# Optimization experiments

Measured on AMD Instinct MI355X. Metric: run time of the kernel, lower is better.

Reference implementation:

```python
import jax, jax.numpy as jnp
import numpy as np

N_NODES = 50000
N_EDGES = 800000
IN_FEATS = 256
OUT_FEATS = 64


def setup_inputs() -> dict:
    key = jax.random.key(0)
    k1, k2, k3, k4 = jax.random.split(key, 4)
    feat = jax.random.normal(k1, (N_NODES, IN_FEATS), dtype=jnp.float32)
    src = jax.random.randint(k2, (N_EDGES,), 0, N_NODES, dtype=jnp.int32)
    dst = jax.random.randint(k3, (N_EDGES,), 0, N_NODES, dtype=jnp.int32)
    # Glorot-uniform like DGL's GraphConv weight init
    limit = float(np.sqrt(6.0 / (IN_FEATS + OUT_FEATS)))
    W = jax.random.uniform(k4, (IN_FEATS, OUT_FEATS), dtype=jnp.float32,
                           minval=-limit, maxval=limit)
    b = jnp.zeros((OUT_FEATS,), dtype=jnp.float32)
    return {"feat": feat, "src": src, "dst": dst, "W": W, "b": b}


def reference(feat, src, dst, W, b):
    n = feat.shape[0]
    ones = jnp.ones_like(src, dtype=feat.dtype)
    out_deg = jax.ops.segment_sum(ones, src, num_segments=n)
    in_deg = jax.ops.segment_sum(ones, dst, num_segments=n)
    # norm='both': deg^{-1/2}, degrees clamped to min 1 (allow_zero_in_degree)
    norm_src = jax.lax.rsqrt(jnp.maximum(out_deg, 1.0))   # [N]
    norm_dst = jax.lax.rsqrt(jnp.maximum(in_deg, 1.0))    # [N]
    # in_feats > out_feats -> apply weight before aggregation (DGL fast path)
    h = (feat * norm_src[:, None]) @ W                    # [N, out]
    agg = jax.ops.segment_sum(h[src], dst, num_segments=n)  # SpMM: sum messages at dst
    rst = agg * norm_dst[:, None] + b
    return jax.nn.sigmoid(rst)
```

## Files before the change

### kernel.cpp

```cpp
#include <hip/hip_runtime.h>
#include <hip/hip_bf16.h>
#include <math.h>

#define N_NODES 50000
#define N_EDGES 800000
#define IN_F 256
#define OUT_F 64

#define BKT 256
#define NB 196
#define CAP 6144
#define PARTA_BLOCKS 400
#define EPB (N_EDGES / PARTA_BLOCKS)
#define GEMM_BM 32

typedef __attribute__((ext_vector_type(8))) short bf16x8;
typedef __attribute__((ext_vector_type(4))) float f32x4;

__device__ __forceinline__ ushort f2bf(float x) {
    __hip_bfloat16 b = __float2bfloat16(x);
    return *reinterpret_cast<ushort*>(&b);
}
__device__ __forceinline__ float bf_lo(uint v) { return __uint_as_float(v << 16); }
__device__ __forceinline__ float bf_hi(uint v) { return __uint_as_float(v & 0xffff0000u); }

__global__ __launch_bounds__(256) void prep_kernel(int* __restrict__ bcnt,
                                                   const float* __restrict__ W,
                                                   ushort* __restrict__ Wpk) {
    const int tid = threadIdx.x;
    if (blockIdx.x == 0) {
        for (int i = tid; i < 2 * NB; i += 256) bcnt[i] = 0;
    } else {
        const int gid = (blockIdx.x - 1) * 256 + tid;
        const int lane = gid & 63;
        const int ct = (gid >> 6) & 3;
        const int step = gid >> 8;
        const int kg = lane >> 4;
        const int n = lane & 15;
        const float* base = W + (size_t)(step * 32 + kg * 8) * OUT_F + ct * 16 + n;
        union { ushort u[8]; uint4 v; } pk;
        #pragma unroll
        for (int j = 0; j < 8; ++j) pk.u[j] = f2bf(base[(size_t)j * OUT_F]);
        ((uint4*)Wpk)[gid] = pk.v;
    }
}

__global__ __launch_bounds__(512) void partA_kernel(const int* __restrict__ src,
                                                    const int* __restrict__ dst,
                                                    int* __restrict__ bcntD,
                                                    int* __restrict__ bcntS,
                                                    uint* __restrict__ pairsD,
                                                    ushort* __restrict__ srcloc) {
    __shared__ int lcntD[NB], lbaseD[NB], lcntS[NB], lbaseS[NB];
    const int tid = threadIdx.x;
    const int n4 = EPB / 4;

    for (int i = tid; i < NB; i += 512) { lcntD[i] = 0; lcntS[i] = 0; }
    __syncthreads();

    const int4* t4 = (const int4*)(dst + (size_t)blockIdx.x * EPB);
    const int4* s4 = (const int4*)(src + (size_t)blockIdx.x * EPB);

    for (int i = tid; i < n4; i += 512) {
        const int4 d = t4[i];
        const int4 s = s4[i];
        atomicAdd(&lcntD[d.x >> 8], 1); atomicAdd(&lcntS[s.x >> 8], 1);
        atomicAdd(&lcntD[d.y >> 8], 1); atomicAdd(&lcntS[s.y >> 8], 1);
        atomicAdd(&lcntD[d.z >> 8], 1); atomicAdd(&lcntS[s.z >> 8], 1);
        atomicAdd(&lcntD[d.w >> 8], 1); atomicAdd(&lcntS[s.w >> 8], 1);
    }
    __syncthreads();

    for (int i = tid; i < NB; i += 512) {
        int c = lcntD[i];
        lbaseD[i] = c ? atomicAdd(&bcntD[i], c) : 0;
        lcntD[i] = 0;
        c = lcntS[i];
        lbaseS[i] = c ? atomicAdd(&bcntS[i], c) : 0;
        lcntS[i] = 0;
    }
    __syncthreads();

    for (int i = tid; i < n4; i += 512) {
        const int4 d = t4[i];
        const int4 s = s4[i];
        int bx, off;
        #define PLACE(dd, ss)                                                  \
            bx = (dd) >> 8; off = atomicAdd(&lcntD[bx], 1);                    \
            pairsD[(size_t)bx * CAP + lbaseD[bx] + off] =                      \
                ((uint)((dd) & 255) << 16) | (uint)(ss);                       \
            bx = (ss) >> 8; off = atomicAdd(&lcntS[bx], 1);                    \
            srcloc[(size_t)bx * CAP + lbaseS[bx] + off] = (ushort)((ss) & 255);
        PLACE(d.x, s.x)
        PLACE(d.y, s.y)
        PLACE(d.z, s.z)
        PLACE(d.w, s.w)
        #undef PLACE
    }
}

__global__ __launch_bounds__(1024) void bucket_kernel(const ushort* __restrict__ srcloc,
                                                      const int* __restrict__ bcntS,
                                                      float* __restrict__ normS,
                                                      const uint* __restrict__ pairsD,
                                                      const int* __restrict__ bcntD,
                                                      int* __restrict__ ptr,
                                                      int* __restrict__ indeg,
                                                      ushort* __restrict__ sorted_src) {
    __shared__ int cnt[BKT];
    __shared__ int loff[BKT];
    __shared__ int wtot[4];
    const int bb = blockIdx.x;
    const int tid = threadIdx.x;
    const int node = bb * BKT + tid;

    if (tid < BKT) cnt[tid] = 0;
    __syncthreads();
    const int nS = bcntS[bb];
    const ushort* sp = srcloc + (size_t)bb * CAP;
    for (int i = tid; i < nS; i += 1024) atomicAdd(&cnt[sp[i]], 1);
    __syncthreads();
    if (tid < BKT && node < N_NODES)
        normS[node] = rsqrtf(fmaxf((float)cnt[tid], 1.0f));
    __syncthreads();

    if (tid < BKT) cnt[tid] = 0;
    __syncthreads();
    const int nD = bcntD[bb];
    const uint* pb = pairsD + (size_t)bb * CAP;
    for (int i = tid; i < nD; i += 1024) atomicAdd(&cnt[pb[i] >> 16], 1);
    __syncthreads();

    if (tid < BKT) {
        const int lane = tid & 63;
        const int wave = tid >> 6;
        const int v = cnt[tid];
        int incl = v;
        #pragma unroll
        for (int d = 1; d < 64; d <<= 1) {
            int u = __shfl_up(incl, d, 64);
            if (lane >= d) incl += u;
        }
        if (lane == 63) wtot[wave] = incl;
        loff[tid] = incl - v;
    }
    __syncthreads();
    if (tid < BKT) {
        const int wave = tid >> 6;
        int woff = 0;
        #pragma unroll
        for (int w = 0; w < 4; ++w)
            if (w < wave) woff += wtot[w];
        const int ex = woff + loff[tid];
        loff[tid] = ex;
        const int v = cnt[tid];
        cnt[tid] = 0;
        if (node < N_NODES) { ptr[node] = bb * CAP + ex; indeg[node] = v; }
    }
    __syncthreads();

    for (int i = tid; i < nD; i += 1024) {
        const uint p = pb[i];
        const int local = (int)(p >> 16);
        const int pos = atomicAdd(&cnt[local], 1);
        sorted_src[(size_t)bb * CAP + loff[local] + pos] = (ushort)(p & 0xFFFFu);
    }
}

__global__ __launch_bounds__(256) void gemm_kernel(const float* __restrict__ feat,
                                                   const ushort* __restrict__ Wpk,
                                                   ushort* __restrict__ h) {
    __shared__ float ftile[GEMM_BM * IN_F];
    const int tid = threadIdx.x;
    const int lane = tid & 63;
    const int wave = tid >> 6;
    const int m = lane & 15;
    const int g = lane >> 4;
    const int rowBase = blockIdx.x * GEMM_BM;
    const char* fb = (const char*)feat;

    #pragma unroll
    for (int it = 0; it < 8; ++it) {
        const int R = it * 4 + wave;
        const int off = (lane * 16) ^ ((R & 7) << 4);
        int grow = rowBase + R;
        if (grow >= N_NODES) grow = N_NODES - 1;
        __builtin_amdgcn_global_load_lds(
            (const __attribute__((address_space(1))) void*)(fb + ((size_t)grow << 10) + off),
            (__attribute__((address_space(3))) void*)((char*)ftile + it * 4096 + wave * 1024),
            16, 0, 0);
    }
    __syncthreads();

    const int rowHalf = wave & 1;
    const int colHalf = wave >> 1;

    f32x4 acc[2];
    acc[0] = (f32x4){0.f, 0.f, 0.f, 0.f};
    acc[1] = (f32x4){0.f, 0.f, 0.f, 0.f};

    const int Rr = rowHalf * 16 + m;
    const int swz = (Rr & 7) << 4;
    const char* rowb = (const char*)ftile + (Rr << 10);
    const bf16x8* wp = (const bf16x8*)Wpk;

    #pragma unroll
    for (int step = 0; step < 8; ++step) {
        const int kb = step * 128 + g * 32;
        const float4 a0 = *(const float4*)(rowb + (kb ^ swz));
        const float4 a1 = *(const float4*)(rowb + ((kb + 16) ^ swz));
        bf16x8 aa;
        aa[0] = (short)f2bf(a0.x); aa[1] = (short)f2bf(a0.y);
        aa[2] = (short)f2bf(a0.z); aa[3] = (short)f2bf(a0.w);
        aa[4] = (short)f2bf(a1.x); aa[5] = (short)f2bf(a1.y);
        aa[6] = (short)f2bf(a1.z); aa[7] = (short)f2bf(a1.w);
        #pragma unroll
        for (int ct = 0; ct < 2; ++ct)
            acc[ct] = __builtin_amdgcn_mfma_f32_16x16x32_bf16(
                aa, wp[(step * 4 + colHalf * 2 + ct) * 64 + lane], acc[ct], 0, 0, 0);
    }

    #pragma unroll
    for (int j = 0; j < 4; ++j) {
        const int row = rowBase + rowHalf * 16 + g * 4 + j;
        if (row < N_NODES) {
            #pragma unroll
            for (int ct = 0; ct < 2; ++ct)
                h[(size_t)row * OUT_F + colHalf * 32 + ct * 16 + m] = f2bf(acc[ct][j]);
        }
    }
}

__global__ __launch_bounds__(256) void gather_kernel(const int* __restrict__ ptr,
                                                     const int* __restrict__ indeg,
                                                     const ushort* __restrict__ sorted_src,
                                                     const float* __restrict__ normS,
                                                     const ushort* __restrict__ h,
                                                     const float* __restrict__ b,
                                                     float* __restrict__ out) {
    const int lane = threadIdx.x & 63;
    const int q = lane & 15;
    const int g = lane >> 4;
    int nid = (int)((blockIdx.x * (size_t)blockDim.x + threadIdx.x) >> 6);
    if (nid >= N_NODES) return;
    nid = __builtin_amdgcn_readfirstlane(nid);

    const int beg = ptr[nid];
    const int deg = indeg[nid];

    float a0 = 0.f, a1 = 0.f, a2 = 0.f, a3 = 0.f;
    const int nfull = deg >> 2;
    int e = beg + g;
    #pragma unroll 4
    for (int i = 0; i < nfull; ++i) {
        const int s = (int)sorted_src[e];
        e += 4;
        const float ns = normS[s];
        const uint2 v = *(const uint2*)(h + (size_t)s * OUT_F + q * 4);
        a0 = fmaf(ns, bf_lo(v.x), a0); a1 = fmaf(ns, bf_hi(v.x), a1);
        a2 = fmaf(ns, bf_lo(v.y), a2); a3 = fmaf(ns, bf_hi(v.y), a3);
    }
    const int rem = deg & 3;
    if (g < rem) {
        const int s = (int)sorted_src[beg + (deg & ~3) + g];
        const float ns = normS[s];
        const uint2 v = *(const uint2*)(h + (size_t)s * OUT_F + q * 4);
        a0 = fmaf(ns, bf_lo(v.x), a0); a1 = fmaf(ns, bf_hi(v.x), a1);
        a2 = fmaf(ns, bf_lo(v.y), a2); a3 = fmaf(ns, bf_hi(v.y), a3);
    }
    a0 += __shfl_xor(a0, 16, 64); a1 += __shfl_xor(a1, 16, 64);
    a2 += __shfl_xor(a2, 16, 64); a3 += __shfl_xor(a3, 16, 64);
    a0 += __shfl_xor(a0, 32, 64); a1 += __shfl_xor(a1, 32, 64);
    a2 += __shfl_xor(a2, 32, 64); a3 += __shfl_xor(a3, 32, 64);

    if (g == 0) {
        const float norm = rsqrtf(fmaxf((float)deg, 1.0f));
        const float4 bb = *(const float4*)(b + q * 4);
        float4 o;
        o.x = 1.0f / (1.0f + expf(-(a0 * norm + bb.x)));
        o.y = 1.0f / (1.0f + expf(-(a1 * norm + bb.y)));
        o.z = 1.0f / (1.0f + expf(-(a2 * norm + bb.z)));
        o.w = 1.0f / (1.0f + expf(-(a3 * norm + bb.w)));
        *(float4*)(out + (size_t)nid * OUT_F + q * 4) = o;
    }
}

extern "C" void kernel_launch(void* const* d_in, const int* in_sizes, int n_in,
                              void* d_out, int out_size, void* d_ws, size_t ws_size,
                              hipStream_t stream) {
    const float* feat = (const float*)d_in[0];
    const int* src    = (const int*)d_in[1];
    const int* dst    = (const int*)d_in[2];
    const float* W    = (const float*)d_in[3];
    const float* b    = (const float*)d_in[4];
    float* out = (float*)d_out;

    char* ws = (char*)d_ws;
    size_t off = 0;
    ushort* h = (ushort*)(ws + off);        off += (size_t)N_NODES * OUT_F * 2;
    float* normS = (float*)(ws + off);      off += (size_t)N_NODES * 4;
    int* indeg = (int*)(ws + off);          off += (size_t)N_NODES * 4;
    int* ptr = (int*)(ws + off);            off += (size_t)N_NODES * 4;
    int* bcnt = (int*)(ws + off);           off += (size_t)2 * NB * 4;
    ushort* Wpk = (ushort*)(ws + off);      off += (size_t)IN_F * OUT_F * 2;
    uint* pairsD = (uint*)(ws + off);       off += (size_t)NB * CAP * 4;
    ushort* srcloc = (ushort*)(ws + off);   off += (size_t)NB * CAP * 2;
    ushort* sorted_src = (ushort*)(ws + off); off += (size_t)NB * CAP * 2;
    int* bcntD = bcnt;
    int* bcntS = bcnt + NB;

    prep_kernel<<<9, 256, 0, stream>>>(bcnt, W, Wpk);

    partA_kernel<<<PARTA_BLOCKS, 512, 0, stream>>>(src, dst, bcntD, bcntS, pairsD, srcloc);

    bucket_kernel<<<NB, 1024, 0, stream>>>(srcloc, bcntS, normS,
                                           pairsD, bcntD, ptr, indeg, sorted_src);

    gemm_kernel<<<(N_NODES + GEMM_BM - 1) / GEMM_BM, 256, 0, stream>>>(feat, Wpk, h);

    gather_kernel<<<(N_NODES * 64 + 255) / 256, 256, 0, stream>>>(
        ptr, indeg, sorted_src, normS, h, b, out);
}
```

Before: 79.03 us.

## Stage edge partition in LDS to coalesce bucketed global writes

The partition kernel now caches each block's edges in shared memory instead of re-reading them from global memory. It computes per-bucket local offsets with a wave prefix scan and places entries into an LDS staging area sorted by bucket. A final pass then writes them out so consecutive threads store contiguous runs within each bucket, replacing scattered global stores. LDS use grows considerably (about 2000 edges times 14 bytes per block), which may lower occupancy.

```diff
diff --git a/kernel.cpp b/kernel.cpp
--- a/kernel.cpp
+++ b/kernel.cpp
@@ -51,19 +51,30 @@
                                                     int* __restrict__ bcntS,
                                                     uint* __restrict__ pairsD,
                                                     ushort* __restrict__ srcloc) {
-    __shared__ int lcntD[NB], lbaseD[NB], lcntS[NB], lbaseS[NB];
+    __shared__ int2 ed[EPB];
+    __shared__ uint stgD[EPB];
+    __shared__ ushort bktD[EPB];
+    __shared__ ushort stgS[EPB];
+    __shared__ ushort bktS[EPB];
+    __shared__ int lcntD[256], lcntS[256];
+    __shared__ int ldofD[256], ldofS[256];
+    __shared__ int lbaseD[NB], lbaseS[NB];
+    __shared__ int wtotD[4], wtotS[4];
     const int tid = threadIdx.x;
     const int n4 = EPB / 4;
 
-    for (int i = tid; i < NB; i += 512) { lcntD[i] = 0; lcntS[i] = 0; }
+    for (int i = tid; i < 256; i += 512) { lcntD[i] = 0; lcntS[i] = 0; }
     __syncthreads();
 
     const int4* t4 = (const int4*)(dst + (size_t)blockIdx.x * EPB);
     const int4* s4 = (const int4*)(src + (size_t)blockIdx.x * EPB);
-
     for (int i = tid; i < n4; i += 512) {
         const int4 d = t4[i];
         const int4 s = s4[i];
+        ed[4 * i + 0] = (int2){d.x, s.x};
+        ed[4 * i + 1] = (int2){d.y, s.y};
+        ed[4 * i + 2] = (int2){d.z, s.z};
+        ed[4 * i + 3] = (int2){d.w, s.w};
         atomicAdd(&lcntD[d.x >> 8], 1); atomicAdd(&lcntS[s.x >> 8], 1);
         atomicAdd(&lcntD[d.y >> 8], 1); atomicAdd(&lcntS[s.y >> 8], 1);
         atomicAdd(&lcntD[d.z >> 8], 1); atomicAdd(&lcntS[s.z >> 8], 1);
@@ -72,30 +83,61 @@
     __syncthreads();
 
     for (int i = tid; i < NB; i += 512) {
-        int c = lcntD[i];
-        lbaseD[i] = c ? atomicAdd(&bcntD[i], c) : 0;
-        lcntD[i] = 0;
-        c = lcntS[i];
-        lbaseS[i] = c ? atomicAdd(&bcntS[i], c) : 0;
-        lcntS[i] = 0;
-    }
-    __syncthreads();
-
-    for (int i = tid; i < n4; i += 512) {
-        const int4 d = t4[i];
-        const int4 s = s4[i];
-        int bx, off;
-        #define PLACE(dd, ss)                                                  \
-            bx = (dd) >> 8; off = atomicAdd(&lcntD[bx], 1);                    \
-            pairsD[(size_t)bx * CAP + lbaseD[bx] + off] =                      \
-                ((uint)((dd) & 255) << 16) | (uint)(ss);                       \
-            bx = (ss) >> 8; off = atomicAdd(&lcntS[bx], 1);                    \
-            srcloc[(size_t)bx * CAP + lbaseS[bx] + off] = (ushort)((ss) & 255);
-        PLACE(d.x, s.x)
-        PLACE(d.y, s.y)
-        PLACE(d.z, s.z)
-        PLACE(d.w, s.w)
-        #undef PLACE
+        const int cD = lcntD[i];
+        lbaseD[i] = cD ? atomicAdd(&bcntD[i], cD) : 0;
+        const int cS = lcntS[i];
+        lbaseS[i] = cS ? atomicAdd(&bcntS[i], cS) : 0;
+    }
+
+    if (tid < 256) {
+        const int lane = tid & 63;
+        const int wave = tid >> 6;
+        const int vD = lcntD[tid], vS = lcntS[tid];
+        int iD = vD, iS = vS;
+        #pragma unroll
+        for (int d = 1; d < 64; d <<= 1) {
+            const int uD = __shfl_up(iD, d, 64);
+            const int uS = __shfl_up(iS, d, 64);
+            if (lane >= d) { iD += uD; iS += uS; }
+        }
+        if (lane == 63) { wtotD[wave] = iD; wtotS[wave] = iS; }
+        ldofD[tid] = iD - vD;
+        ldofS[tid] = iS - vS;
+    }
+    __syncthreads();
+    if (tid < 256) {
+        const int wave = tid >> 6;
+        int woD = 0, woS = 0;
+        #pragma unroll
+        for (int w = 0; w < 4; ++w)
+            if (w < wave) { woD += wtotD[w]; woS += wtotS[w]; }
+        ldofD[tid] += woD;
+        ldofS[tid] += woS;
+        lcntD[tid] = 0;
+        lcntS[tid] = 0;
+    }
+    __syncthreads();
+
+    for (int i = tid; i < EPB; i += 512) {
+        const int2 e = ed[i];
+        int bx = e.x >> 8;
+        int pos = atomicAdd(&lcntD[bx], 1);
+        int sl = ldofD[bx] + pos;
+        stgD[sl] = ((uint)(e.x & 255) << 16) | (uint)e.y;
+        bktD[sl] = (ushort)bx;
+        bx = e.y >> 8;
+        pos = atomicAdd(&lcntS[bx], 1);
+        sl = ldofS[bx] + pos;
+        stgS[sl] = (ushort)(e.y & 255);
+        bktS[sl] = (ushort)bx;
+    }
+    __syncthreads();
+
+    for (int i = tid; i < EPB; i += 512) {
+        int b = bktD[i];
+        pairsD[(size_t)b * CAP + lbaseD[b] + (i - ldofD[b])] = stgD[i];
+        b = bktS[i];
+        srcloc[(size_t)b * CAP + lbaseS[b] + (i - ldofS[b])] = stgS[i];
     }
 }
 
```

Result: faster. 75.40 us (-4.6%).
